# Performance work log

Hardware: AMD Instinct MI355X
Metric: run time of the kernel (lower is better)

Reference implementation:

```python
import jax, jax.numpy as jnp
import numpy as np

WINDOW = 11
C1 = 0.01 ** 2
C2 = 0.03 ** 2
PAD = WINDOW // 2


def _box_filter(img, kernel):
    # img: [B,1,H,W], kernel: [1,1,w,w]; SAME padding (odd window)
    return jax.lax.conv_general_dilated(
        img, kernel,
        window_strides=(1, 1),
        padding=[(PAD, PAD), (PAD, PAD)],
        dimension_numbers=('NCHW', 'OIHW', 'NCHW'))


def setup_inputs() -> dict:
    key = jax.random.key(0)
    kx, ky = jax.random.split(key)
    B, C, H, W = 64, 1, 512, 512
    x = jax.random.uniform(kx, (B, C, H, W), dtype=jnp.float32)
    y = jax.random.uniform(ky, (B, C, H, W), dtype=jnp.float32)
    kernel = jnp.ones((1, 1, WINDOW, WINDOW), dtype=jnp.float32) / (WINDOW ** 2)
    return {"x": x, "y": y, "kernel": kernel}


def reference(x, y, kernel):
    mu_x = _box_filter(x, kernel)
    mu_y = _box_filter(y, kernel)
    mu_x2 = mu_x * mu_x
    mu_y2 = mu_y * mu_y
    mu_xy = mu_x * mu_y
    sigma_x2 = _box_filter(x * x, kernel) - mu_x2
    sigma_y2 = _box_filter(y * y, kernel) - mu_y2
    sigma_xy = _box_filter(x * y, kernel) - mu_xy
    ssim_map = ((2.0 * mu_xy + C1) * (2.0 * sigma_xy + C2)) / (
        (mu_x2 + mu_y2 + C1) * (sigma_x2 + sigma_y2 + C2))
    return 1.0 - jnp.mean(ssim_map)
```

## Files before the change

kernel.cpp:

```cpp
#include <hip/hip_runtime.h>
#include <stdint.h>


#define IMG_H 512
#define IMG_W 512
#define N_IMG 64
#define RAD   5
#define SH    8
#define WAVES 8
#define NBANDG 8
#define NBLOCKS (N_IMG * NBANDG)

#define C1_SSIM 1.0e-4f
#define C2_SSIM 9.0e-4f

#define SLOT_BYTES 4096

typedef __attribute__((address_space(3))) uint32_t lds_u32_t;
typedef const __attribute__((address_space(1))) uint32_t glb_u32_t;

__device__ __forceinline__ void dma16(void* lds, const void* g) {
    __builtin_amdgcn_global_load_lds((glb_u32_t*)g, (lds_u32_t*)lds, 16, 0, 0);
}

__global__ __launch_bounds__(512) void ssim_fused(const float* __restrict__ x,
                                                  const float* __restrict__ y,
                                                  float* __restrict__ part)
{
    __shared__ __align__(16) char ring[WAVES][2][SLOT_BYTES];

    const int tx  = threadIdx.x & 63;
    const int ts  = threadIdx.x >> 6;

    const int wid = (blockIdx.x & 7) * (NBLOCKS / 8) + (blockIdx.x >> 3);
    const int img = wid >> 3;
    const int bg  = wid & (NBANDG - 1);
    const int r0  = bg * (WAVES * SH) + ts * SH;
    const int c0  = tx * 8;

    const float* __restrict__ xi = x + (size_t)img * (IMG_H * IMG_W);
    const float* __restrict__ yi = y + (size_t)img * (IMG_H * IMG_W);

    auto dma_row = [&](char* s, int ri) -> float {
        int rc = ri < 0 ? 0 : (ri > IMG_H - 1 ? IMG_H - 1 : ri);
        float sc = (ri >= 0 && ri < IMG_H) ? 1.0f : 0.0f;
        const char* xg = (const char*)(xi + (size_t)rc * IMG_W) + tx * 16;
        const char* yg = (const char*)(yi + (size_t)rc * IMG_W) + tx * 16;
        dma16(s,        xg);
        dma16(s + 1024, xg + 1024);
        dma16(s + 2048, yg);
        dma16(s + 3072, yg + 1024);
        return sc;
    };

    float Vx[8], Vy[8], Vss[8], Vxy[8];
#pragma unroll
    for (int j = 0; j < 8; ++j) { Vx[j] = 0.f; Vy[j] = 0.f; Vss[j] = 0.f; Vxy[j] = 0.f; }

    auto accum_lds = [&](const char* s, float f) {
        const float4* xr = (const float4*)(s + (size_t)tx * 32);
        const float4* yr = (const float4*)(s + 2048 + (size_t)tx * 32);
        float4 x0 = xr[0], x1 = xr[1];
        float4 y0 = yr[0], y1 = yr[1];
        float xs[8] = {x0.x, x0.y, x0.z, x0.w, x1.x, x1.y, x1.z, x1.w};
        float ys[8] = {y0.x, y0.y, y0.z, y0.w, y1.x, y1.y, y1.z, y1.w};
#pragma unroll
        for (int j = 0; j < 8; ++j) {
            float fx = f * xs[j];
            float fy = f * ys[j];
            Vx[j] += fx;
            Vy[j] += fy;
            Vss[j] = fmaf(fx, xs[j], Vss[j]);
            Vss[j] = fmaf(fy, ys[j], Vss[j]);
            Vxy[j] = fmaf(fx, ys[j], Vxy[j]);
        }
    };

    auto hsum = [&](const float (&V)[8], float (&S)[8]) {
        float w[18];
#pragma unroll
        for (int k = 0; k < 5; ++k) {
            float l = __shfl_up(V[3 + k], 1, 64);
            w[k] = (tx == 0) ? 0.f : l;
        }
#pragma unroll
        for (int j = 0; j < 8; ++j) w[5 + j] = V[j];
#pragma unroll
        for (int k = 0; k < 5; ++k) {
            float r = __shfl_down(V[k], 1, 64);
            w[13 + k] = (tx == 63) ? 0.f : r;
        }
        float s = 0.f;
#pragma unroll
        for (int t = 0; t < 11; ++t) s += w[t];
        S[0] = s;
#pragma unroll
        for (int j = 1; j < 8; ++j) { s += w[j + 10] - w[j - 1]; S[j] = s; }
    };

    char* cur = &ring[ts][0][0];
    char* nxt = &ring[ts][1][0];

    float scCur = dma_row(cur, r0 - 5);
#pragma unroll 1
    for (int i = 0; i < 2 * RAD; ++i) {
        accum_lds(cur, scCur);
        float scN = dma_row(nxt, r0 - 4 + i);
        char* t = cur; cur = nxt; nxt = t;
        scCur = scN;
    }

    const float inv121 = 1.0f / 121.0f;
    float loss = 0.0f;

#pragma unroll 1
    for (int ro = r0; ro < r0 + SH; ++ro) {
        accum_lds(cur, scCur);
        float scN = dma_row(nxt, ro + 6);

        int  rs      = ro - RAD;
        bool haveSub = (rs >= 0);
        float4 sx0, sx1, sy0, sy1;
        if (haveSub) {
            const float4* xr = (const float4*)(xi + (size_t)rs * IMG_W + c0);
            const float4* yr = (const float4*)(yi + (size_t)rs * IMG_W + c0);
            sx0 = xr[0]; sx1 = xr[1]; sy0 = yr[0]; sy1 = yr[1];
        }

        float Sx[8], Sy[8], Sss[8], Sxy[8];
        hsum(Vx,  Sx);
        hsum(Vy,  Sy);
        hsum(Vss, Sss);
        hsum(Vxy, Sxy);

#pragma unroll
        for (int j = 0; j < 8; ++j) {
            float mx  = Sx[j] * inv121;
            float my  = Sy[j] * inv121;
            float mx2 = mx * mx;
            float my2 = my * my;
            float mxy = mx * my;
            float vs  = Sss[j] * inv121 - mx2 - my2;
            float vxy = Sxy[j] * inv121 - mxy;
            float num = (2.0f * mxy + C1_SSIM) * (2.0f * vxy + C2_SSIM);
            float den = (mx2 + my2 + C1_SSIM) * (vs + C2_SSIM);
            loss += __fdividef(num, den);
        }

        if (haveSub) {
            float xs[8] = {sx0.x, sx0.y, sx0.z, sx0.w, sx1.x, sx1.y, sx1.z, sx1.w};
            float ys[8] = {sy0.x, sy0.y, sy0.z, sy0.w, sy1.x, sy1.y, sy1.z, sy1.w};
#pragma unroll
            for (int j = 0; j < 8; ++j) {
                Vx[j]  -= xs[j];
                Vy[j]  -= ys[j];
                Vss[j] = fmaf(-xs[j], xs[j], Vss[j]);
                Vss[j] = fmaf(-ys[j], ys[j], Vss[j]);
                Vxy[j] = fmaf(-xs[j], ys[j], Vxy[j]);
            }
        }

        char* t = cur; cur = nxt; nxt = t;
        scCur = scN;
    }

#pragma unroll
    for (int off = 32; off > 0; off >>= 1)
        loss += __shfl_down(loss, off, 64);

    __syncthreads();
    float* pr = reinterpret_cast<float*>(&ring[0][0][0]);
    if (tx == 0) pr[ts] = loss;
    __syncthreads();
    if (threadIdx.x == 0) {
        float t = ((pr[0] + pr[1]) + (pr[2] + pr[3]))
                + ((pr[4] + pr[5]) + (pr[6] + pr[7]));
        part[blockIdx.x] = t;
    }
}

__global__ __launch_bounds__(256) void ssim_reduce(const float* __restrict__ part,
                                                   float* __restrict__ out)
{
    const int t  = threadIdx.x;
    const int tx = t & 63;
    float s = part[t] + part[t + 256];
#pragma unroll
    for (int off = 32; off > 0; off >>= 1)
        s += __shfl_down(s, off, 64);
    __shared__ float ws[4];
    if (tx == 0) ws[t >> 6] = s;
    __syncthreads();
    if (t == 0) {
        float total = (ws[0] + ws[1]) + (ws[2] + ws[3]);
        out[0] = 1.0f - total * (1.0f / ((float)N_IMG * IMG_H * IMG_W));
    }
}

extern "C" void kernel_launch(void* const* d_in, const int* in_sizes, int n_in,
                              void* d_out, int out_size, void* d_ws, size_t ws_size,
                              hipStream_t stream) {
    const float* x = (const float*)d_in[0];
    const float* y = (const float*)d_in[1];
    float* part = (float*)d_ws;

    ssim_fused<<<NBLOCKS, 512, 0, stream>>>(x, y, part);
    ssim_reduce<<<1, 256, 0, stream>>>(part, (float*)d_out);
}
```

Before: 183.7 us.

## Use single-wave blocks with tall row bands and LDS ring for subtraction

```diff
diff --git a/kernel.cpp b/kernel.cpp
--- a/kernel.cpp
+++ b/kernel.cpp
@@ -6,10 +6,10 @@
 #define IMG_W 512
 #define N_IMG 64
 #define RAD   5
-#define SH    8
-#define WAVES 8
+#define SH    64
 #define NBANDG 8
 #define NBLOCKS (N_IMG * NBANDG)
+#define NSLOT 13
 
 #define C1_SSIM 1.0e-4f
 #define C2_SSIM 9.0e-4f
@@ -23,41 +23,38 @@
     __builtin_amdgcn_global_load_lds((glb_u32_t*)g, (lds_u32_t*)lds, 16, 0, 0);
 }
 
-__global__ __launch_bounds__(512) void ssim_fused(const float* __restrict__ x,
-                                                  const float* __restrict__ y,
-                                                  float* __restrict__ part)
+__global__ __launch_bounds__(64) void ssim_fused(const float* __restrict__ x,
+                                                 const float* __restrict__ y,
+                                                 float* __restrict__ part)
 {
-    __shared__ __align__(16) char ring[WAVES][2][SLOT_BYTES];
+    __shared__ __align__(16) char ring[NSLOT][SLOT_BYTES];
 
-    const int tx  = threadIdx.x & 63;
-    const int ts  = threadIdx.x >> 6;
+    const int tx  = threadIdx.x;
 
     const int wid = (blockIdx.x & 7) * (NBLOCKS / 8) + (blockIdx.x >> 3);
     const int img = wid >> 3;
     const int bg  = wid & (NBANDG - 1);
-    const int r0  = bg * (WAVES * SH) + ts * SH;
-    const int c0  = tx * 8;
+    const int r0  = bg * SH;
 
     const float* __restrict__ xi = x + (size_t)img * (IMG_H * IMG_W);
     const float* __restrict__ yi = y + (size_t)img * (IMG_H * IMG_W);
 
-    auto dma_row = [&](char* s, int ri) -> float {
+    auto dma_row = [&](int slot, int ri) {
         int rc = ri < 0 ? 0 : (ri > IMG_H - 1 ? IMG_H - 1 : ri);
-        float sc = (ri >= 0 && ri < IMG_H) ? 1.0f : 0.0f;
+        char* s = &ring[slot][0];
         const char* xg = (const char*)(xi + (size_t)rc * IMG_W) + tx * 16;
         const char* yg = (const char*)(yi + (size_t)rc * IMG_W) + tx * 16;
         dma16(s,        xg);
         dma16(s + 1024, xg + 1024);
         dma16(s + 2048, yg);
         dma16(s + 3072, yg + 1024);
-        return sc;
     };
 
     float Vx[8], Vy[8], Vss[8], Vxy[8];
 #pragma unroll
     for (int j = 0; j < 8; ++j) { Vx[j] = 0.f; Vy[j] = 0.f; Vss[j] = 0.f; Vxy[j] = 0.f; }
 
-    auto accum_lds = [&](const char* s, float f) {
+    auto accum_add = [&](const char* s, float f) {
         const float4* xr = (const float4*)(s + (size_t)tx * 32);
         const float4* yr = (const float4*)(s + 2048 + (size_t)tx * 32);
         float4 x0 = xr[0], x1 = xr[1];
@@ -73,6 +70,23 @@
             Vss[j] = fmaf(fx, xs[j], Vss[j]);
             Vss[j] = fmaf(fy, ys[j], Vss[j]);
             Vxy[j] = fmaf(fx, ys[j], Vxy[j]);
+        }
+    };
+
+    auto accum_sub = [&](const char* s) {
+        const float4* xr = (const float4*)(s + (size_t)tx * 32);
+        const float4* yr = (const float4*)(s + 2048 + (size_t)tx * 32);
+        float4 x0 = xr[0], x1 = xr[1];
+        float4 y0 = yr[0], y1 = yr[1];
+        float xs[8] = {x0.x, x0.y, x0.z, x0.w, x1.x, x1.y, x1.z, x1.w};
+        float ys[8] = {y0.x, y0.y, y0.z, y0.w, y1.x, y1.y, y1.z, y1.w};
+#pragma unroll
+        for (int j = 0; j < 8; ++j) {
+            Vx[j]  -= xs[j];
+            Vy[j]  -= ys[j];
+            Vss[j] = fmaf(-xs[j], xs[j], Vss[j]);
+            Vss[j] = fmaf(-ys[j], ys[j], Vss[j]);
+            Vxy[j] = fmaf(-xs[j], ys[j], Vxy[j]);
         }
     };
 
@@ -98,34 +112,27 @@
         for (int j = 1; j < 8; ++j) { s += w[j + 10] - w[j - 1]; S[j] = s; }
     };
 
-    char* cur = &ring[ts][0][0];
-    char* nxt = &ring[ts][1][0];
-
-    float scCur = dma_row(cur, r0 - 5);
 #pragma unroll 1
-    for (int i = 0; i < 2 * RAD; ++i) {
-        accum_lds(cur, scCur);
-        float scN = dma_row(nxt, r0 - 4 + i);
-        char* t = cur; cur = nxt; nxt = t;
-        scCur = scN;
+    for (int i = 0; i < 11; ++i) dma_row(i, r0 - RAD + i);
+#pragma unroll 1
+    for (int i = 0; i < 10; ++i) {
+        int ri = r0 - RAD + i;
+        accum_add(&ring[i][0], ri >= 0 ? 1.0f : 0.0f);
     }
 
     const float inv121 = 1.0f / 121.0f;
     float loss = 0.0f;
+    int sAdd = 10, sSub = 12, sPre = 11;
+    const int subLo = (r0 > 0) ? (r0 - RAD) : 0;
 
 #pragma unroll 1
-    for (int ro = r0; ro < r0 + SH; ++ro) {
-        accum_lds(cur, scCur);
-        float scN = dma_row(nxt, ro + 6);
+    for (int r = r0; r < r0 + SH; ++r) {
+        accum_add(&ring[sAdd][0], (r + RAD < IMG_H) ? 1.0f : 0.0f);
 
-        int  rs      = ro - RAD;
-        bool haveSub = (rs >= 0);
-        float4 sx0, sx1, sy0, sy1;
-        if (haveSub) {
-            const float4* xr = (const float4*)(xi + (size_t)rs * IMG_W + c0);
-            const float4* yr = (const float4*)(yi + (size_t)rs * IMG_W + c0);
-            sx0 = xr[0]; sx1 = xr[1]; sy0 = yr[0]; sy1 = yr[1];
-        }
+        int rs = r - RAD - 1;
+        if (rs >= subLo) accum_sub(&ring[sSub][0]);
+
+        if (r < r0 + SH - 1) dma_row(sPre, r + RAD + 1);
 
         float Sx[8], Sy[8], Sss[8], Sxy[8];
         hsum(Vx,  Sx);
@@ -147,36 +154,16 @@
             loss += __fdividef(num, den);
         }
 
-        if (haveSub) {
-            float xs[8] = {sx0.x, sx0.y, sx0.z, sx0.w, sx1.x, sx1.y, sx1.z, sx1.w};
-            float ys[8] = {sy0.x, sy0.y, sy0.z, sy0.w, sy1.x, sy1.y, sy1.z, sy1.w};
-#pragma unroll
-            for (int j = 0; j < 8; ++j) {
-                Vx[j]  -= xs[j];
-                Vy[j]  -= ys[j];
-                Vss[j] = fmaf(-xs[j], xs[j], Vss[j]);
-                Vss[j] = fmaf(-ys[j], ys[j], Vss[j]);
-                Vxy[j] = fmaf(-xs[j], ys[j], Vxy[j]);
-            }
-        }
-
-        char* t = cur; cur = nxt; nxt = t;
-        scCur = scN;
+        if (++sAdd == NSLOT) sAdd = 0;
+        if (++sSub == NSLOT) sSub = 0;
+        if (++sPre == NSLOT) sPre = 0;
     }
 
 #pragma unroll
     for (int off = 32; off > 0; off >>= 1)
         loss += __shfl_down(loss, off, 64);
-
-    __syncthreads();
-    float* pr = reinterpret_cast<float*>(&ring[0][0][0]);
-    if (tx == 0) pr[ts] = loss;
-    __syncthreads();
-    if (threadIdx.x == 0) {
-        float t = ((pr[0] + pr[1]) + (pr[2] + pr[3]))
-                + ((pr[4] + pr[5]) + (pr[6] + pr[7]));
-        part[blockIdx.x] = t;
-    }
+    if (tx == 0)
+        part[blockIdx.x] = loss;
 }
 
 __global__ __launch_bounds__(256) void ssim_reduce(const float* __restrict__ part,
@@ -204,6 +191,6 @@
     const float* y = (const float*)d_in[1];
     float* part = (float*)d_ws;
 
-    ssim_fused<<<NBLOCKS, 512, 0, stream>>>(x, y, part);
+    ssim_fused<<<NBLOCKS, 64, 0, stream>>>(x, y, part);
     ssim_reduce<<<1, 256, 0, stream>>>(part, (float*)d_out);
 }
```

Result: slower. 192.6 us (+4.9%).
